# Kernel tuning notes

Measured on AMD Instinct MI355X. Metric: run time of the kernel, lower is better.

The kernel has to match this reference:

```python
import jax, jax.numpy as jnp
import numpy as np

DIM = 4096
N_HEAD = 32
N_LOCAL = 32
HEAD_DIM = 128
INTER = 11008
EPS = 1e-5
THRESH = 0.05  # thresh_q/k/v/o/gate/up/down (all equal here)
SEQ = 1
B = 1
ROPE_BASE = 10000.0


def _precompute_freqs_cis(seq_len, n_elem, base=ROPE_BASE):
    freqs = 1.0 / base ** (np.arange(0, n_elem, 2)[: n_elem // 2].astype(np.float32) / n_elem)
    f = np.outer(np.arange(seq_len, dtype=np.float32), freqs)
    return jnp.asarray(np.stack([np.cos(f), np.sin(f)], axis=-1), dtype=jnp.float32)  # [S, D/2, 2]


def setup_inputs() -> dict:
    key = jax.random.key(0)
    ks = jax.random.split(key, 7)
    s = 0.02
    return {
        "x": jax.random.normal(ks[0], (B, SEQ, DIM), jnp.float32),
        "freqs_cis": _precompute_freqs_cis(SEQ, HEAD_DIM),
        "wqkv": jax.random.normal(ks[1], ((N_HEAD + 2 * N_LOCAL) * HEAD_DIM, DIM), jnp.float32) * s,
        "wo": jax.random.normal(ks[2], (DIM, DIM), jnp.float32) * s,
        "w1": jax.random.normal(ks[3], (INTER, DIM), jnp.float32) * s,
        "w2": jax.random.normal(ks[4], (DIM, INTER), jnp.float32) * s,
        "w3": jax.random.normal(ks[5], (INTER, DIM), jnp.float32) * s,
        "attn_norm_w": jnp.ones((DIM,), jnp.float32),
        "ffn_norm_w": jnp.ones((DIM,), jnp.float32),
        "mask": jnp.ones((1, 1, SEQ, SEQ), jnp.bool_),
    }


def _rmsnorm(x, w):
    return x * jax.lax.rsqrt(jnp.mean(x * x, axis=-1, keepdims=True) + EPS) * w


def _splitk(x, A, thresh):
    # simulate_splitk: Y[b,s] = A @ (x[b,s] * (|x[b,s]| > thresh))  when seq_len == 1
    # (the original's seq_len > 1 branch uses unmasked X)
    if x.shape[1] == 1:
        x = jnp.where(jnp.abs(x) > thresh, x, jnp.zeros((), x.dtype))
    return jnp.einsum("bsz,nz->bsn", x, A)


def _rope(x, fc):
    # x: [B,S,H,D], fc: [S, D/2, 2] (cos, sin), interleaved pairs
    xr = x.reshape(*x.shape[:-1], HEAD_DIM // 2, 2)
    fc = fc.reshape(1, x.shape[1], 1, HEAD_DIM // 2, 2)
    o0 = xr[..., 0] * fc[..., 0] - xr[..., 1] * fc[..., 1]
    o1 = xr[..., 1] * fc[..., 0] + xr[..., 0] * fc[..., 1]
    return jnp.stack([o0, o1], axis=-1).reshape(x.shape)


def _sdpa(q, k, v, mask):
    # q,k,v: [B,H,S,D]; mask: [1,1,S,S] bool
    scale = 1.0 / np.sqrt(HEAD_DIM)
    scores = jnp.einsum("bhqd,bhkd->bhqk", q, k) * scale
    scores = jnp.where(mask, scores, jnp.asarray(-1e30, scores.dtype))
    return jnp.einsum("bhqk,bhkd->bhqd", jax.nn.softmax(scores, axis=-1), v)


def reference(x, freqs_cis, wqkv, wo, w1, w2, w3, attn_norm_w, ffn_norm_w, mask):
    bsz, seqlen, _ = x.shape
    kv_size = N_LOCAL * HEAD_DIM
    # --- attention ---
    h_in = _rmsnorm(x, attn_norm_w)
    q0, k0, v0 = wqkv[:kv_size], wqkv[kv_size:2 * kv_size], wqkv[2 * kv_size:]
    q = _splitk(h_in, q0, THRESH).reshape(bsz, seqlen, N_HEAD, HEAD_DIM)
    k = _splitk(h_in, k0, THRESH).reshape(bsz, seqlen, N_LOCAL, HEAD_DIM)
    v = _splitk(h_in, v0, THRESH).reshape(bsz, seqlen, N_LOCAL, HEAD_DIM)
    q = _rope(q, freqs_cis).transpose(0, 2, 1, 3)  # [B,H,S,D]
    k = _rope(k, freqs_cis).transpose(0, 2, 1, 3)
    v = v.transpose(0, 2, 1, 3)
    rep = N_HEAD // N_LOCAL
    if rep > 1:
        k = jnp.repeat(k, rep, axis=1)
        v = jnp.repeat(v, rep, axis=1)
    y = _sdpa(q, k, v, mask).transpose(0, 2, 1, 3).reshape(bsz, seqlen, DIM)
    y = _splitk(y, wo, THRESH)
    h = x + y
    # --- SwiGLU FFN ---
    hf = _rmsnorm(h, ffn_norm_w)
    gate = _splitk(hf, w1, THRESH)
    up = _splitk(hf, w3, THRESH)
    down = _splitk(jax.nn.silu(gate) * up, w2, THRESH)
    return h + down
```

## Files before the change

### kernel.cpp

```cpp
#include <hip/hip_runtime.h>
#include <math.h>

#define DIM 4096
#define INTER 11008
#define EPS 1e-5f
#define THRESH 0.05f

__device__ __forceinline__ float wave_sum(float v) {
#pragma unroll
    for (int off = 32; off > 0; off >>= 1) v += __shfl_xor(v, off, 64);
    return v;
}

__global__ __launch_bounds__(1024) void rmsnorm_thr_kernel(
        const float* __restrict__ x, const float* __restrict__ w,
        float* __restrict__ out) {
    __shared__ float red[16];
    __shared__ float s_scale;
    const int tid = threadIdx.x;
    float4 xv = reinterpret_cast<const float4*>(x)[tid];
    float ss = xv.x * xv.x + xv.y * xv.y + xv.z * xv.z + xv.w * xv.w;
    ss = wave_sum(ss);
    const int wid = tid >> 6, lane = tid & 63;
    if (lane == 0) red[wid] = ss;
    __syncthreads();
    if (tid == 0) {
        float s = 0.f;
#pragma unroll
        for (int i = 0; i < 16; ++i) s += red[i];
        s_scale = rsqrtf(s / (float)DIM + EPS);
    }
    __syncthreads();
    const float scale = s_scale;
    float4 wv = reinterpret_cast<const float4*>(w)[tid];
    float4 o;
    o.x = xv.x * scale * wv.x;
    o.y = xv.y * scale * wv.y;
    o.z = xv.z * scale * wv.z;
    o.w = xv.w * scale * wv.w;
    o.x = (fabsf(o.x) > THRESH) ? o.x : 0.f;
    o.y = (fabsf(o.y) > THRESH) ? o.y : 0.f;
    o.z = (fabsf(o.z) > THRESH) ? o.z : 0.f;
    o.w = (fabsf(o.w) > THRESH) ? o.w : 0.f;
    reinterpret_cast<float4*>(out)[tid] = o;
}

__global__ __launch_bounds__(256) void gemv_thr_kernel(
        const float* __restrict__ W, const float* __restrict__ x,
        float* __restrict__ out) {
    const int lane = threadIdx.x & 63;
    const int row = (blockIdx.x << 2) + (threadIdx.x >> 6);
    const float* wr = W + (size_t)row * DIM;
    float acc = 0.f;
#pragma unroll 4
    for (int k = 0; k < DIM; k += 256) {
        float4 wv = *reinterpret_cast<const float4*>(wr + k + (lane << 2));
        float4 xv = *reinterpret_cast<const float4*>(x + k + (lane << 2));
        acc = fmaf(wv.x, xv.x, acc);
        acc = fmaf(wv.y, xv.y, acc);
        acc = fmaf(wv.z, xv.z, acc);
        acc = fmaf(wv.w, xv.w, acc);
    }
    acc = wave_sum(acc);
    if (lane == 0) out[row] = (fabsf(acc) > THRESH) ? acc : 0.f;
}

__global__ __launch_bounds__(256) void gemv_res_kernel(
        const float* __restrict__ W, const float* __restrict__ x,
        const float* __restrict__ res, float* __restrict__ out) {
    const int lane = threadIdx.x & 63;
    const int row = (blockIdx.x << 2) + (threadIdx.x >> 6);
    const float* wr = W + (size_t)row * DIM;
    float acc = 0.f;
#pragma unroll 4
    for (int k = 0; k < DIM; k += 256) {
        float4 wv = *reinterpret_cast<const float4*>(wr + k + (lane << 2));
        float4 xv = *reinterpret_cast<const float4*>(x + k + (lane << 2));
        acc = fmaf(wv.x, xv.x, acc);
        acc = fmaf(wv.y, xv.y, acc);
        acc = fmaf(wv.z, xv.z, acc);
        acc = fmaf(wv.w, xv.w, acc);
    }
    acc = wave_sum(acc);
    if (lane == 0) out[row] = res[row] + acc;
}

__global__ __launch_bounds__(256) void gateup_kernel(
        const float* __restrict__ W1, const float* __restrict__ W3,
        const float* __restrict__ x, float* __restrict__ out) {
    const int lane = threadIdx.x & 63;
    const int row = (blockIdx.x << 2) + (threadIdx.x >> 6);
    const float* w1r = W1 + (size_t)row * DIM;
    const float* w3r = W3 + (size_t)row * DIM;
    float g = 0.f, u = 0.f;
#pragma unroll 4
    for (int k = 0; k < DIM; k += 256) {
        float4 xv = *reinterpret_cast<const float4*>(x + k + (lane << 2));
        float4 av = *reinterpret_cast<const float4*>(w1r + k + (lane << 2));
        float4 bv = *reinterpret_cast<const float4*>(w3r + k + (lane << 2));
        g = fmaf(av.x, xv.x, g);
        g = fmaf(av.y, xv.y, g);
        g = fmaf(av.z, xv.z, g);
        g = fmaf(av.w, xv.w, g);
        u = fmaf(bv.x, xv.x, u);
        u = fmaf(bv.y, xv.y, u);
        u = fmaf(bv.z, xv.z, u);
        u = fmaf(bv.w, xv.w, u);
    }
    g = wave_sum(g);
    u = wave_sum(u);
    if (lane == 0) {
        float s = g / (1.f + expf(-g));
        float a = s * u;
        out[row] = (fabsf(a) > THRESH) ? a : 0.f;
    }
}

__global__ __launch_bounds__(256) void down_kernel(
        const float* __restrict__ W2, const float* __restrict__ x,
        const float* __restrict__ h, float* __restrict__ out) {
    const int lane = threadIdx.x & 63;
    const int row = (blockIdx.x << 2) + (threadIdx.x >> 6);
    const float* wr = W2 + (size_t)row * INTER;
    float acc = 0.f;
#pragma unroll 4
    for (int k = 0; k < INTER; k += 256) {
        float4 wv = *reinterpret_cast<const float4*>(wr + k + (lane << 2));
        float4 xv = *reinterpret_cast<const float4*>(x + k + (lane << 2));
        acc = fmaf(wv.x, xv.x, acc);
        acc = fmaf(wv.y, xv.y, acc);
        acc = fmaf(wv.z, xv.z, acc);
        acc = fmaf(wv.w, xv.w, acc);
    }
    acc = wave_sum(acc);
    if (lane == 0) out[row] = h[row] + acc;
}

extern "C" void kernel_launch(void* const* d_in, const int* in_sizes, int n_in,
                              void* d_out, int out_size, void* d_ws, size_t ws_size,
                              hipStream_t stream) {
    const float* x    = (const float*)d_in[0];
    const float* wqkv = (const float*)d_in[2];
    const float* wo   = (const float*)d_in[3];
    const float* w1   = (const float*)d_in[4];
    const float* w2   = (const float*)d_in[5];
    const float* w3   = (const float*)d_in[6];
    const float* anw  = (const float*)d_in[7];
    const float* fnw  = (const float*)d_in[8];
    float* out = (float*)d_out;

    float* ws   = (float*)d_ws;
    float* hs   = ws;
    float* vt   = ws + 4096;
    float* h    = ws + 8192;
    float* hft  = ws + 12288;
    float* actt = ws + 16384;

    const float* wv = wqkv + (size_t)2 * 4096 * DIM;

    rmsnorm_thr_kernel<<<1, 1024, 0, stream>>>(x, anw, hs);
    gemv_thr_kernel  <<<DIM / 4, 256, 0, stream>>>(wv, hs, vt);
    gemv_res_kernel  <<<DIM / 4, 256, 0, stream>>>(wo, vt, x, h);
    rmsnorm_thr_kernel<<<1, 1024, 0, stream>>>(h, fnw, hft);
    gateup_kernel    <<<INTER / 4, 256, 0, stream>>>(w1, w3, hft, actt);
    down_kernel      <<<DIM / 4, 256, 0, stream>>>(w2, actt, h, out);
}
```

Measured before the change: 139.4 us.

## Fuse RMSNorm and threshold into the following GEMVs, add multi-accumulator loops

Removes the two single-block RMSNorm launches. Each wave now recomputes the norm scale from the 16KB input vector and applies the weight and threshold inline before its dot product. All GEMV loops also use several independent accumulators, which adds memory-level parallelism. This saves two launches and their serial single-block latency, at the cost of redundant per-wave reads of x and the norm weights, which should mostly hit in cache.

Result: faster. 132.9 us (-4.7%).

```diff
diff --git a/kernel.cpp b/kernel.cpp
--- a/kernel.cpp
+++ b/kernel.cpp
@@ -12,57 +12,53 @@
     return v;
 }
 
-__global__ __launch_bounds__(1024) void rmsnorm_thr_kernel(
-        const float* __restrict__ x, const float* __restrict__ w,
-        float* __restrict__ out) {
-    __shared__ float red[16];
-    __shared__ float s_scale;
-    const int tid = threadIdx.x;
-    float4 xv = reinterpret_cast<const float4*>(x)[tid];
-    float ss = xv.x * xv.x + xv.y * xv.y + xv.z * xv.z + xv.w * xv.w;
+__device__ __forceinline__ float wave_rms_scale(const float* __restrict__ x,
+                                                int lane) {
+    float ss = 0.f;
+#pragma unroll
+    for (int k = 0; k < DIM; k += 256) {
+        float4 v = *reinterpret_cast<const float4*>(x + k + (lane << 2));
+        ss = fmaf(v.x, v.x, ss);
+        ss = fmaf(v.y, v.y, ss);
+        ss = fmaf(v.z, v.z, ss);
+        ss = fmaf(v.w, v.w, ss);
+    }
     ss = wave_sum(ss);
-    const int wid = tid >> 6, lane = tid & 63;
-    if (lane == 0) red[wid] = ss;
-    __syncthreads();
-    if (tid == 0) {
-        float s = 0.f;
-#pragma unroll
-        for (int i = 0; i < 16; ++i) s += red[i];
-        s_scale = rsqrtf(s / (float)DIM + EPS);
-    }
-    __syncthreads();
-    const float scale = s_scale;
-    float4 wv = reinterpret_cast<const float4*>(w)[tid];
-    float4 o;
-    o.x = xv.x * scale * wv.x;
-    o.y = xv.y * scale * wv.y;
-    o.z = xv.z * scale * wv.z;
-    o.w = xv.w * scale * wv.w;
-    o.x = (fabsf(o.x) > THRESH) ? o.x : 0.f;
-    o.y = (fabsf(o.y) > THRESH) ? o.y : 0.f;
-    o.z = (fabsf(o.z) > THRESH) ? o.z : 0.f;
-    o.w = (fabsf(o.w) > THRESH) ? o.w : 0.f;
-    reinterpret_cast<float4*>(out)[tid] = o;
+    return rsqrtf(ss * (1.f / (float)DIM) + EPS);
 }
 
-__global__ __launch_bounds__(256) void gemv_thr_kernel(
+__device__ __forceinline__ float thr(float v) {
+    return (fabsf(v) > THRESH) ? v : 0.f;
+}
+
+__global__ __launch_bounds__(256) void gemv_rms_thr_kernel(
         const float* __restrict__ W, const float* __restrict__ x,
-        float* __restrict__ out) {
+        const float* __restrict__ nw, float* __restrict__ out) {
     const int lane = threadIdx.x & 63;
     const int row = (blockIdx.x << 2) + (threadIdx.x >> 6);
+    const float scale = wave_rms_scale(x, lane);
     const float* wr = W + (size_t)row * DIM;
-    float acc = 0.f;
-#pragma unroll 4
-    for (int k = 0; k < DIM; k += 256) {
-        float4 wv = *reinterpret_cast<const float4*>(wr + k + (lane << 2));
-        float4 xv = *reinterpret_cast<const float4*>(x + k + (lane << 2));
-        acc = fmaf(wv.x, xv.x, acc);
-        acc = fmaf(wv.y, xv.y, acc);
-        acc = fmaf(wv.z, xv.z, acc);
-        acc = fmaf(wv.w, xv.w, acc);
+    float acc[4] = {0.f, 0.f, 0.f, 0.f};
+    for (int k = 0; k < DIM; k += 1024) {
+#pragma unroll
+        for (int u = 0; u < 4; ++u) {
+            const int kk = k + (u << 8) + (lane << 2);
+            float4 wv = *reinterpret_cast<const float4*>(wr + kk);
+            float4 xv = *reinterpret_cast<const float4*>(x + kk);
+            float4 nv = *reinterpret_cast<const float4*>(nw + kk);
+            float x0 = thr(xv.x * scale * nv.x);
+            float x1 = thr(xv.y * scale * nv.y);
+            float x2 = thr(xv.z * scale * nv.z);
+            float x3 = thr(xv.w * scale * nv.w);
+            acc[u] = fmaf(wv.x, x0, acc[u]);
+            acc[u] = fmaf(wv.y, x1, acc[u]);
+            acc[u] = fmaf(wv.z, x2, acc[u]);
+            acc[u] = fmaf(wv.w, x3, acc[u]);
+        }
     }
-    acc = wave_sum(acc);
-    if (lane == 0) out[row] = (fabsf(acc) > THRESH) ? acc : 0.f;
+    float a = (acc[0] + acc[1]) + (acc[2] + acc[3]);
+    a = wave_sum(a);
+    if (lane == 0) out[row] = thr(a);
 }
 
 __global__ __launch_bounds__(256) void gemv_res_kernel(
@@ -71,48 +67,61 @@
     const int lane = threadIdx.x & 63;
     const int row = (blockIdx.x << 2) + (threadIdx.x >> 6);
     const float* wr = W + (size_t)row * DIM;
-    float acc = 0.f;
-#pragma unroll 4
-    for (int k = 0; k < DIM; k += 256) {
-        float4 wv = *reinterpret_cast<const float4*>(wr + k + (lane << 2));
-        float4 xv = *reinterpret_cast<const float4*>(x + k + (lane << 2));
-        acc = fmaf(wv.x, xv.x, acc);
-        acc = fmaf(wv.y, xv.y, acc);
-        acc = fmaf(wv.z, xv.z, acc);
-        acc = fmaf(wv.w, xv.w, acc);
+    float acc[4] = {0.f, 0.f, 0.f, 0.f};
+    for (int k = 0; k < DIM; k += 1024) {
+#pragma unroll
+        for (int u = 0; u < 4; ++u) {
+            const int kk = k + (u << 8) + (lane << 2);
+            float4 wv = *reinterpret_cast<const float4*>(wr + kk);
+            float4 xv = *reinterpret_cast<const float4*>(x + kk);
+            acc[u] = fmaf(wv.x, xv.x, acc[u]);
+            acc[u] = fmaf(wv.y, xv.y, acc[u]);
+            acc[u] = fmaf(wv.z, xv.z, acc[u]);
+            acc[u] = fmaf(wv.w, xv.w, acc[u]);
+        }
     }
-    acc = wave_sum(acc);
-    if (lane == 0) out[row] = res[row] + acc;
+    float a = (acc[0] + acc[1]) + (acc[2] + acc[3]);
+    a = wave_sum(a);
+    if (lane == 0) out[row] = res[row] + a;
 }
 
-__global__ __launch_bounds__(256) void gateup_kernel(
+__global__ __launch_bounds__(256) void gateup_rms_kernel(
         const float* __restrict__ W1, const float* __restrict__ W3,
-        const float* __restrict__ x, float* __restrict__ out) {
+        const float* __restrict__ h, const float* __restrict__ nw,
+        float* __restrict__ out) {
     const int lane = threadIdx.x & 63;
     const int row = (blockIdx.x << 2) + (threadIdx.x >> 6);
+    const float scale = wave_rms_scale(h, lane);
     const float* w1r = W1 + (size_t)row * DIM;
     const float* w3r = W3 + (size_t)row * DIM;
-    float g = 0.f, u = 0.f;
-#pragma unroll 4
-    for (int k = 0; k < DIM; k += 256) {
-        float4 xv = *reinterpret_cast<const float4*>(x + k + (lane << 2));
-        float4 av = *reinterpret_cast<const float4*>(w1r + k + (lane << 2));
-        float4 bv = *reinterpret_cast<const float4*>(w3r + k + (lane << 2));
-        g = fmaf(av.x, xv.x, g);
-        g = fmaf(av.y, xv.y, g);
-        g = fmaf(av.z, xv.z, g);
-        g = fmaf(av.w, xv.w, g);
-        u = fmaf(bv.x, xv.x, u);
-        u = fmaf(bv.y, xv.y, u);
-        u = fmaf(bv.z, xv.z, u);
-        u = fmaf(bv.w, xv.w, u);
+    float g[2] = {0.f, 0.f}, u[2] = {0.f, 0.f};
+    for (int k = 0; k < DIM; k += 512) {
+#pragma unroll
+        for (int p = 0; p < 2; ++p) {
+            const int kk = k + (p << 8) + (lane << 2);
+            float4 hv = *reinterpret_cast<const float4*>(h + kk);
+            float4 nv = *reinterpret_cast<const float4*>(nw + kk);
+            float4 av = *reinterpret_cast<const float4*>(w1r + kk);
+            float4 bv = *reinterpret_cast<const float4*>(w3r + kk);
+            float x0 = thr(hv.x * scale * nv.x);
+            float x1 = thr(hv.y * scale * nv.y);
+            float x2 = thr(hv.z * scale * nv.z);
+            float x3 = thr(hv.w * scale * nv.w);
+            g[p] = fmaf(av.x, x0, g[p]);
+            g[p] = fmaf(av.y, x1, g[p]);
+            g[p] = fmaf(av.z, x2, g[p]);
+            g[p] = fmaf(av.w, x3, g[p]);
+            u[p] = fmaf(bv.x, x0, u[p]);
+            u[p] = fmaf(bv.y, x1, u[p]);
+            u[p] = fmaf(bv.z, x2, u[p]);
+            u[p] = fmaf(bv.w, x3, u[p]);
+        }
     }
-    g = wave_sum(g);
-    u = wave_sum(u);
+    float gg = wave_sum(g[0] + g[1]);
+    float uu = wave_sum(u[0] + u[1]);
     if (lane == 0) {
-        float s = g / (1.f + expf(-g));
-        float a = s * u;
-        out[row] = (fabsf(a) > THRESH) ? a : 0.f;
+        float s = gg / (1.f + expf(-gg));
+        out[row] = thr(s * uu);
     }
 }
 
@@ -122,18 +131,33 @@
     const int lane = threadIdx.x & 63;
     const int row = (blockIdx.x << 2) + (threadIdx.x >> 6);
     const float* wr = W2 + (size_t)row * INTER;
-    float acc = 0.f;
-#pragma unroll 4
-    for (int k = 0; k < INTER; k += 256) {
-        float4 wv = *reinterpret_cast<const float4*>(wr + k + (lane << 2));
-        float4 xv = *reinterpret_cast<const float4*>(x + k + (lane << 2));
-        acc = fmaf(wv.x, xv.x, acc);
-        acc = fmaf(wv.y, xv.y, acc);
-        acc = fmaf(wv.z, xv.z, acc);
-        acc = fmaf(wv.w, xv.w, acc);
+    float acc[4] = {0.f, 0.f, 0.f, 0.f};
+    int k = 0;
+    for (; k + 1024 <= INTER; k += 1024) {
+#pragma unroll
+        for (int u = 0; u < 4; ++u) {
+            const int kk = k + (u << 8) + (lane << 2);
+            float4 wv = *reinterpret_cast<const float4*>(wr + kk);
+            float4 xv = *reinterpret_cast<const float4*>(x + kk);
+            acc[u] = fmaf(wv.x, xv.x, acc[u]);
+            acc[u] = fmaf(wv.y, xv.y, acc[u]);
+            acc[u] = fmaf(wv.z, xv.z, acc[u]);
+            acc[u] = fmaf(wv.w, xv.w, acc[u]);
+        }
     }
-    acc = wave_sum(acc);
-    if (lane == 0) out[row] = h[row] + acc;
+#pragma unroll
+    for (int u = 0; u < 3; ++u) {
+        const int kk = k + (u << 8) + (lane << 2);
+        float4 wv = *reinterpret_cast<const float4*>(wr + kk);
+        float4 xv = *reinterpret_cast<const float4*>(x + kk);
+        acc[u] = fmaf(wv.x, xv.x, acc[u]);
+        acc[u] = fmaf(wv.y, xv.y, acc[u]);
+        acc[u] = fmaf(wv.z, xv.z, acc[u]);
+        acc[u] = fmaf(wv.w, xv.w, acc[u]);
+    }
+    float a = (acc[0] + acc[1]) + (acc[2] + acc[3]);
+    a = wave_sum(a);
+    if (lane == 0) out[row] = h[row] + a;
 }
 
 extern "C" void kernel_launch(void* const* d_in, const int* in_sizes, int n_in,
@@ -150,18 +174,14 @@
     float* out = (float*)d_out;
 
     float* ws   = (float*)d_ws;
-    float* hs   = ws;
-    float* vt   = ws + 4096;
-    float* h    = ws + 8192;
-    float* hft  = ws + 12288;
-    float* actt = ws + 16384;
+    float* vt   = ws;
+    float* h    = ws + 4096;
+    float* actt = ws + 8192;
 
     const float* wv = wqkv + (size_t)2 * 4096 * DIM;
 
-    rmsnorm_thr_kernel<<<1, 1024, 0, stream>>>(x, anw, hs);
-    gemv_thr_kernel  <<<DIM / 4, 256, 0, stream>>>(wv, hs, vt);
-    gemv_res_kernel  <<<DIM / 4, 256, 0, stream>>>(wo, vt, x, h);
-    rmsnorm_thr_kernel<<<1, 1024, 0, stream>>>(h, fnw, hft);
-    gateup_kernel    <<<INTER / 4, 256, 0, stream>>>(w1, w3, hft, actt);
-    down_kernel      <<<DIM / 4, 256, 0, stream>>>(w2, actt, h, out);
+    gemv_rms_thr_kernel<<<DIM / 4, 256, 0, stream>>>(wv, x, anw, vt);
+    gemv_res_kernel    <<<DIM / 4, 256, 0, stream>>>(wo, vt, x, h);
+    gateup_rms_kernel  <<<INTER / 4, 256, 0, stream>>>(w1, w3, h, fnw, actt);
+    down_kernel        <<<DIM / 4, 256, 0, stream>>>(w2, actt, h, out);
 }
```
